# Kernel tuning notes

Hardware: AMD Instinct MI355X
Metric: run time of the kernel (lower is better)

## Reference

```python
import jax, jax.numpy as jnp
import numpy as np

B, C, H, W, K = 8, 256, 128, 128, 9
P = K // 2
DN = ('NCHW', 'OIHW', 'NCHW')


def _dw(x, w, pad):
    # depthwise conv: w has shape (C,1,kh,kw), feature_group_count=C
    return jax.lax.conv_general_dilated(
        x, w, window_strides=(1, 1), padding=pad,
        dimension_numbers=DN, feature_group_count=C)


def setup_inputs() -> dict:
    key = jax.random.key(0)
    ks = jax.random.split(key, 6)
    s = 1.0 / np.sqrt(K)
    return {
        'x': jax.random.normal(ks[0], (B, C, H, W), dtype=jnp.float32),
        'wh1': jax.random.normal(ks[1], (C, 1, 1, K), dtype=jnp.float32) * s,
        'wh2': jax.random.normal(ks[2], (C, 1, 1, K), dtype=jnp.float32) * s,
        'wv1': jax.random.normal(ks[3], (C, 1, K, 1), dtype=jnp.float32) * s,
        'wv2': jax.random.normal(ks[4], (C, 1, K, 1), dtype=jnp.float32) * s,
        'wproj': jax.random.normal(ks[5], (C, 4 * C), dtype=jnp.float32) / np.sqrt(4 * C),
    }


def reference(x, wh1, wh2, wv1, wv2, wproj):
    pad_h = ((0, 0), (P, P))  # 1xK conv pads width
    pad_v = ((P, P), (0, 0))  # Kx1 conv pads height
    y = jnp.concatenate([
        _dw(x, wh1, pad_h),
        _dw(x, wh2, pad_h),
        _dw(x, wv1, pad_v),
        _dw(x, wv2, pad_v),
    ], axis=1)  # (B, 4C, H, W)
    out = jnp.einsum('oc,bchw->bohw', wproj, y)  # 1x1 projection
    return jax.nn.relu(out)
```

## Files before the change

kernel.cpp:

```cpp
#include <hip/hip_runtime.h>
#include <hip/hip_bf16.h>

#define BB 8
#define CC 256
#define HH 128
#define WW 128
#define KS 9
#define NPIX (BB*HH*WW)
#define KDIM (4*CC)

#define XROW   2176
#define XT2_CG 295936
#define XT2_B  4734976
#define XT2_BYTES 75759616u

typedef __attribute__((ext_vector_type(8))) short bf16x8;
typedef __attribute__((ext_vector_type(4))) float f32x4;

static __device__ __forceinline__ unsigned short f2bf(float f) {
  union { float f; unsigned u; } v; v.f = f;
  unsigned r = v.u + 0x7FFF + ((v.u >> 16) & 1);
  return (unsigned short)(r >> 16);
}
static __device__ __forceinline__ float bf2f(unsigned short u) {
  union { unsigned u; float f; } v; v.u = ((unsigned)u) << 16;
  return v.f;
}

static __device__ __forceinline__ void gload_lds16(const void* g, void* l) {
  __builtin_amdgcn_global_load_lds(
      (const __attribute__((address_space(1))) void*)g,
      (__attribute__((address_space(3))) void*)l, 16, 0, 0);
}

__global__ void zero_kernel(uint4* __restrict__ p, long n16) {
  long i = (long)blockIdx.x * blockDim.x + threadIdx.x;
  long stride = (long)gridDim.x * blockDim.x;
  uint4 z = make_uint4(0, 0, 0, 0);
  for (; i < n16; i += stride) p[i] = z;
}

__global__ void prep_kernel(const float* __restrict__ wproj,
                            unsigned short* __restrict__ Ap) {
  int idx = blockIdx.x * 256 + threadIdx.x;
  int o  = idx >> 10;
  int kp = idx & 1023;
  int c  = kp >> 2;
  int t  = kp & 3;
  Ap[idx] = f2bf(wproj[o * 1024 + t * 256 + c]);
}

__global__ void wprep_kernel(const float* __restrict__ wh1,
                             const float* __restrict__ wh2,
                             const float* __restrict__ wv1,
                             const float* __restrict__ wv2,
                             float* __restrict__ wt) {
  int idx = blockIdx.x * 256 + threadIdx.x;
  int c = idx & 255;
  int q = idx >> 8;
  int cv = q / 9, k = q % 9;
  const float* src = (cv == 0) ? wh1 : (cv == 1) ? wh2 : (cv == 2) ? wv1 : wv2;
  wt[idx] = src[c * KS + k];
}

__global__ __launch_bounds__(256)
void transpose_kernel(const float* __restrict__ x,
                      unsigned short* __restrict__ xt2) {
  __shared__ float lds[64][65];
  int g   = blockIdx.x;
  int wt_ = g & 1;
  int h   = (g >> 1) & 127;
  int ct  = (g >> 8) & 3;
  int b   = g >> 10;
  int w0  = wt_ * 64;
  int tid = threadIdx.x;

  const float* xin = x + ((size_t)(b * 256 + ct * 64) << 14) + h * 128 + w0;
  int ci = tid >> 4;
  int w4 = (tid & 15) * 4;
#pragma unroll
  for (int i = 0; i < 4; ++i) {
    int c_ = ci + i * 16;
    float4 v = *(const float4*)(xin + ((size_t)c_ << 14) + w4);
    lds[c_][w4 + 0] = v.x; lds[c_][w4 + 1] = v.y;
    lds[c_][w4 + 2] = v.z; lds[c_][w4 + 3] = v.w;
  }
  __syncthreads();

  int wl  = (tid >> 6) * 16 + ((tid & 63) >> 2);
  int cl4 = (tid & 3) * 4;
#pragma unroll
  for (int g2 = 0; g2 < 4; ++g2) {
    ushort4 o;
    o.x = f2bf(lds[g2 * 16 + cl4 + 0][wl]);
    o.y = f2bf(lds[g2 * 16 + cl4 + 1][wl]);
    o.z = f2bf(lds[g2 * 16 + cl4 + 2][wl]);
    o.w = f2bf(lds[g2 * 16 + cl4 + 3][wl]);
    size_t dst = (size_t)b * XT2_B + (size_t)(ct * 4 + g2) * XT2_CG
               + (size_t)(h + 4) * XROW + (size_t)(w0 + wl + 4) * 16 + cl4;
    *(ushort4*)(xt2 + dst) = o;
  }
}

__global__ __launch_bounds__(512, 4)
void fused_kernel(const unsigned short* __restrict__ Ap,
                  const unsigned short* __restrict__ xt2,
                  const float* __restrict__ wt,
                  float* __restrict__ out) {
  __shared__ __align__(16) short Xs[9 * XROW];
  __shared__ __align__(16) short Bs[128 * 64];

  int bid = blockIdx.x;
  int pt  = (bid & 7) * 128 + (bid >> 3);
  int b   = pt >> 7, h = pt & 127;
  int tid = threadIdx.x;
  int lane = tid & 63;
  int wv  = tid >> 6;
  int om  = wv & 3, pn = wv >> 2;
  int l15 = lane & 15, kseg = lane >> 4;

  int cl = tid & 15;
  int wq = tid >> 4;

  const short* A  = (const short*)Ap;
  const short* xb = (const short*)xt2 + (size_t)b * XT2_B + (size_t)h * XROW;

  f32x4 acc[4][4] = {};

  for (int cg = 0; cg < 16; ++cg) {
    const char* src = (const char*)(xb + (size_t)cg * XT2_CG);
#pragma unroll
    for (int i = 0; i < 5; ++i) {
      int off = i * 8192 + tid * 16;
      if (off < 9 * XROW * 2)
        gload_lds16(src + off, (char*)Xs + off);
    }
    __syncthreads();

    bf16x8 af[2][4];
#pragma unroll
    for (int kk = 0; kk < 2; ++kk) {
      int kg = cg * 64 + kk * 32 + kseg * 8;
#pragma unroll
      for (int m = 0; m < 4; ++m)
        af[kk][m] = *(const bf16x8*)(A + (size_t)(om * 64 + m * 16 + l15) * KDIM + kg);
    }

    int c = cg * 16 + cl;
    float s[4][4];
#pragma unroll
    for (int dw = 0; dw < 4; ++dw)
#pragma unroll
      for (int t = 0; t < 4; ++t) s[dw][t] = 0.f;
#pragma unroll
    for (int j = 0; j < KS; ++j) {
      float w1 = wt[(0 * KS + j) * CC + c];
      float w2 = wt[(1 * KS + j) * CC + c];
      float w3 = wt[(2 * KS + j) * CC + c];
      float w4 = wt[(3 * KS + j) * CC + c];
#pragma unroll
      for (int dw = 0; dw < 4; ++dw) {
        int w = wq * 4 + dw;
        float xh = bf2f((unsigned short)Xs[4 * XROW + (w + j) * 16 + cl]);
        float xv = bf2f((unsigned short)Xs[j * XROW + (w + 4) * 16 + cl]);
        s[dw][0] = fmaf(xh, w1, s[dw][0]);
        s[dw][1] = fmaf(xh, w2, s[dw][1]);
        s[dw][2] = fmaf(xv, w3, s[dw][2]);
        s[dw][3] = fmaf(xv, w4, s[dw][3]);
      }
    }
#pragma unroll
    for (int dw = 0; dw < 4; ++dw) {
      int w = wq * 4 + dw;
      unsigned u0 = (unsigned)f2bf(s[dw][0]) | ((unsigned)f2bf(s[dw][1]) << 16);
      unsigned u1 = (unsigned)f2bf(s[dw][2]) | ((unsigned)f2bf(s[dw][3]) << 16);
      int byt = (w * 128 + cl * 8) ^ ((w & 7) << 4);
      *(uint2*)((char*)Bs + byt) = make_uint2(u0, u1);
    }
    __syncthreads();

#pragma unroll
    for (int kk = 0; kk < 2; ++kk) {
      bf16x8 bfr[4];
#pragma unroll
      for (int n = 0; n < 4; ++n) {
        int row = pn * 64 + n * 16 + l15;
        int byt = (row * 128 + kk * 64 + kseg * 16) ^ ((row & 7) << 4);
        bfr[n] = *(const bf16x8*)((const char*)Bs + byt);
      }
#pragma unroll
      for (int m = 0; m < 4; ++m)
#pragma unroll
        for (int n = 0; n < 4; ++n)
          acc[m][n] = __builtin_amdgcn_mfma_f32_16x16x32_bf16(af[kk][m], bfr[n],
                                                              acc[m][n], 0, 0, 0);
    }
    __syncthreads();
  }

  float* Ls = (float*)Xs;
  const int LP = 132;
  int b2 = pt >> 7, h2 = pt & 127;
  int er = tid >> 4;
  int ec = (tid & 15) * 8;
  size_t obase = ((size_t)(b2 * 256) << 14) + (h2 << 7);

#pragma unroll
  for (int oc = 0; oc < 8; ++oc) {
    __syncthreads();
    if (om == (oc >> 1)) {
      int mb = (oc & 1) * 2;
#pragma unroll
      for (int mm = 0; mm < 2; ++mm) {
#pragma unroll
        for (int n = 0; n < 4; ++n) {
#pragma unroll
          for (int r = 0; r < 4; ++r) {
            int row = mm * 16 + kseg * 4 + r;
            int col = pn * 64 + n * 16 + l15;
            Ls[row * LP + col] = acc[mb + mm][n][r];
          }
        }
      }
    }
    __syncthreads();
    float4 v0 = *(const float4*)&Ls[er * LP + ec];
    float4 v1 = *(const float4*)&Ls[er * LP + ec + 4];
    size_t oaddr = obase + ((size_t)(oc * 32 + er) << 14) + ec;
    *(float4*)&out[oaddr] = make_float4(fmaxf(v0.x, 0.f), fmaxf(v0.y, 0.f),
                                        fmaxf(v0.z, 0.f), fmaxf(v0.w, 0.f));
    *(float4*)&out[oaddr + 4] = make_float4(fmaxf(v1.x, 0.f), fmaxf(v1.y, 0.f),
                                            fmaxf(v1.z, 0.f), fmaxf(v1.w, 0.f));
  }
}

extern "C" void kernel_launch(void* const* d_in, const int* in_sizes, int n_in,
                              void* d_out, int out_size, void* d_ws, size_t ws_size,
                              hipStream_t stream) {
  (void)in_sizes; (void)n_in; (void)out_size; (void)ws_size;
  const float* x     = (const float*)d_in[0];
  const float* wh1   = (const float*)d_in[1];
  const float* wh2   = (const float*)d_in[2];
  const float* wv1   = (const float*)d_in[3];
  const float* wv2   = (const float*)d_in[4];
  const float* wproj = (const float*)d_in[5];
  float* out = (float*)d_out;

  char* wsb = (char*)d_ws;
  unsigned short* Xt2 = (unsigned short*)wsb;
  unsigned short* Ap  = (unsigned short*)(wsb + XT2_BYTES);
  float* Wt           = (float*)(wsb + XT2_BYTES + (size_t)CC * KDIM * 2);

  hipLaunchKernelGGL(zero_kernel, dim3(2048), dim3(256), 0, stream,
                     (uint4*)Xt2, (long)(XT2_BYTES / 16));
  hipLaunchKernelGGL(prep_kernel, dim3(1024), dim3(256), 0, stream, wproj, Ap);
  hipLaunchKernelGGL(wprep_kernel, dim3(36), dim3(256), 0, stream,
                     wh1, wh2, wv1, wv2, Wt);
  hipLaunchKernelGGL(transpose_kernel, dim3(8192), dim3(256), 0, stream, x, Xt2);
  hipLaunchKernelGGL(fused_kernel, dim3(1024), dim3(512), 0, stream,
                     Ap, Xt2, Wt, out);
}
```

Baseline: 541.9 us.

## Read fp32 input directly in fused kernel, dropping padded bf16 transpose staging

Removes the zero-fill and transpose kernels that built a padded channel-interleaved bf16 copy of x. The fused kernel now reads x straight from NCHW with float4 loads, handles halo boundaries with per-load bounds checks, and keeps the depthwise weights in LDS in per-channel order. This cuts a full extra pass over the input, the padded workspace writes and two kernel launches. In exchange each block reloads nine rows per channel from global memory through L2 instead of staging them once in LDS, and the per-thread loads are strided across channels, which may lower coalescing.

```diff
diff --git a/kernel.cpp b/kernel.cpp
--- a/kernel.cpp
+++ b/kernel.cpp
@@ -9,11 +9,6 @@
 #define NPIX (BB*HH*WW)
 #define KDIM (4*CC)
 
-#define XROW   2176
-#define XT2_CG 295936
-#define XT2_B  4734976
-#define XT2_BYTES 75759616u
-
 typedef __attribute__((ext_vector_type(8))) short bf16x8;
 typedef __attribute__((ext_vector_type(4))) float f32x4;
 
@@ -21,23 +16,6 @@
   union { float f; unsigned u; } v; v.f = f;
   unsigned r = v.u + 0x7FFF + ((v.u >> 16) & 1);
   return (unsigned short)(r >> 16);
-}
-static __device__ __forceinline__ float bf2f(unsigned short u) {
-  union { unsigned u; float f; } v; v.u = ((unsigned)u) << 16;
-  return v.f;
-}
-
-static __device__ __forceinline__ void gload_lds16(const void* g, void* l) {
-  __builtin_amdgcn_global_load_lds(
-      (const __attribute__((address_space(1))) void*)g,
-      (__attribute__((address_space(3))) void*)l, 16, 0, 0);
-}
-
-__global__ void zero_kernel(uint4* __restrict__ p, long n16) {
-  long i = (long)blockIdx.x * blockDim.x + threadIdx.x;
-  long stride = (long)gridDim.x * blockDim.x;
-  uint4 z = make_uint4(0, 0, 0, 0);
-  for (; i < n16; i += stride) p[i] = z;
 }
 
 __global__ void prep_kernel(const float* __restrict__ wproj,
@@ -54,60 +32,21 @@
                              const float* __restrict__ wh2,
                              const float* __restrict__ wv1,
                              const float* __restrict__ wv2,
-                             float* __restrict__ wt) {
+                             float* __restrict__ wt2) {
   int idx = blockIdx.x * 256 + threadIdx.x;
-  int c = idx & 255;
-  int q = idx >> 8;
-  int cv = q / 9, k = q % 9;
+  int c = idx / 36;
+  int q = idx - c * 36;
+  int cv = q / 9, k = q - cv * 9;
   const float* src = (cv == 0) ? wh1 : (cv == 1) ? wh2 : (cv == 2) ? wv1 : wv2;
-  wt[idx] = src[c * KS + k];
-}
-
-__global__ __launch_bounds__(256)
-void transpose_kernel(const float* __restrict__ x,
-                      unsigned short* __restrict__ xt2) {
-  __shared__ float lds[64][65];
-  int g   = blockIdx.x;
-  int wt_ = g & 1;
-  int h   = (g >> 1) & 127;
-  int ct  = (g >> 8) & 3;
-  int b   = g >> 10;
-  int w0  = wt_ * 64;
-  int tid = threadIdx.x;
-
-  const float* xin = x + ((size_t)(b * 256 + ct * 64) << 14) + h * 128 + w0;
-  int ci = tid >> 4;
-  int w4 = (tid & 15) * 4;
-#pragma unroll
-  for (int i = 0; i < 4; ++i) {
-    int c_ = ci + i * 16;
-    float4 v = *(const float4*)(xin + ((size_t)c_ << 14) + w4);
-    lds[c_][w4 + 0] = v.x; lds[c_][w4 + 1] = v.y;
-    lds[c_][w4 + 2] = v.z; lds[c_][w4 + 3] = v.w;
-  }
-  __syncthreads();
-
-  int wl  = (tid >> 6) * 16 + ((tid & 63) >> 2);
-  int cl4 = (tid & 3) * 4;
-#pragma unroll
-  for (int g2 = 0; g2 < 4; ++g2) {
-    ushort4 o;
-    o.x = f2bf(lds[g2 * 16 + cl4 + 0][wl]);
-    o.y = f2bf(lds[g2 * 16 + cl4 + 1][wl]);
-    o.z = f2bf(lds[g2 * 16 + cl4 + 2][wl]);
-    o.w = f2bf(lds[g2 * 16 + cl4 + 3][wl]);
-    size_t dst = (size_t)b * XT2_B + (size_t)(ct * 4 + g2) * XT2_CG
-               + (size_t)(h + 4) * XROW + (size_t)(w0 + wl + 4) * 16 + cl4;
-    *(ushort4*)(xt2 + dst) = o;
-  }
+  wt2[idx] = src[c * KS + k];
 }
 
 __global__ __launch_bounds__(512, 4)
 void fused_kernel(const unsigned short* __restrict__ Ap,
-                  const unsigned short* __restrict__ xt2,
-                  const float* __restrict__ wt,
+                  const float* __restrict__ x,
+                  const float* __restrict__ wt2,
                   float* __restrict__ out) {
-  __shared__ __align__(16) short Xs[9 * XROW];
+  __shared__ __align__(16) float Ws[256 * 36];
   __shared__ __align__(16) short Bs[128 * 64];
 
   int bid = blockIdx.x;
@@ -119,69 +58,83 @@
   int om  = wv & 3, pn = wv >> 2;
   int l15 = lane & 15, kseg = lane >> 4;
 
-  int cl = tid & 15;
-  int wq = tid >> 4;
-
+  int tc   = tid & 15;
+  int wseg = tid >> 4;
+  int w0   = wseg * 4;
+
+  {
+    const float4* srcw = (const float4*)wt2;
+    float4* dstw = (float4*)Ws;
+    for (int i = tid; i < 2304; i += 512) dstw[i] = srcw[i];
+  }
+  __syncthreads();
+
+  const float* xb = x + ((size_t)b << 22);
   const short* A  = (const short*)Ap;
-  const short* xb = (const short*)xt2 + (size_t)b * XT2_B + (size_t)h * XROW;
 
   f32x4 acc[4][4] = {};
 
   for (int cg = 0; cg < 16; ++cg) {
-    const char* src = (const char*)(xb + (size_t)cg * XT2_CG);
-#pragma unroll
-    for (int i = 0; i < 5; ++i) {
-      int off = i * 8192 + tid * 16;
-      if (off < 9 * XROW * 2)
-        gload_lds16(src + off, (char*)Xs + off);
-    }
-    __syncthreads();
-
-    bf16x8 af[2][4];
+    int c = cg * 16 + tc;
+    const float* xc = xb + ((size_t)c << 14);
+
+    float W[36];
+#pragma unroll
+    for (int i = 0; i < 9; ++i) {
+      float4 v = *(const float4*)&Ws[c * 36 + i * 4];
+      W[i*4+0] = v.x; W[i*4+1] = v.y; W[i*4+2] = v.z; W[i*4+3] = v.w;
+    }
+
+    float xh[12];
+    {
+      const float* xrow = xc + h * WW;
+#pragma unroll
+      for (int sgi = 0; sgi < 3; ++sgi) {
+        int wi = w0 - 4 + sgi * 4;
+        float4 v;
+        if (wi >= 0 && wi <= WW - 4) v = *(const float4*)(xrow + wi);
+        else v = make_float4(0.f, 0.f, 0.f, 0.f);
+        xh[sgi*4+0] = v.x; xh[sgi*4+1] = v.y;
+        xh[sgi*4+2] = v.z; xh[sgi*4+3] = v.w;
+      }
+    }
+
+    float s1[4] = {0.f,0.f,0.f,0.f}, s2[4] = {0.f,0.f,0.f,0.f};
+    float s3[4] = {0.f,0.f,0.f,0.f}, s4[4] = {0.f,0.f,0.f,0.f};
+#pragma unroll
+    for (int j = 0; j < KS; ++j) {
+      int r = h - 4 + j;
+      float4 vj;
+      if (r >= 0 && r < HH) vj = *(const float4*)(xc + r * WW + w0);
+      else vj = make_float4(0.f, 0.f, 0.f, 0.f);
+      float wj1 = W[j], wj2 = W[9+j], wj3 = W[18+j], wj4 = W[27+j];
+#pragma unroll
+      for (int dw = 0; dw < 4; ++dw) {
+        float a = xh[dw + j];
+        float v = (dw == 0) ? vj.x : (dw == 1) ? vj.y : (dw == 2) ? vj.z : vj.w;
+        s1[dw] = fmaf(a, wj1, s1[dw]);
+        s2[dw] = fmaf(a, wj2, s2[dw]);
+        s3[dw] = fmaf(v, wj3, s3[dw]);
+        s4[dw] = fmaf(v, wj4, s4[dw]);
+      }
+    }
+#pragma unroll
+    for (int dw = 0; dw < 4; ++dw) {
+      int w = w0 + dw;
+      unsigned u0 = (unsigned)f2bf(s1[dw]) | ((unsigned)f2bf(s2[dw]) << 16);
+      unsigned u1 = (unsigned)f2bf(s3[dw]) | ((unsigned)f2bf(s4[dw]) << 16);
+      int byt = (w * 128 + tc * 8) ^ ((w & 7) << 4);
+      *(uint2*)((char*)Bs + byt) = make_uint2(u0, u1);
+    }
+    __syncthreads();
+
 #pragma unroll
     for (int kk = 0; kk < 2; ++kk) {
+      bf16x8 af[4], bfr[4];
       int kg = cg * 64 + kk * 32 + kseg * 8;
 #pragma unroll
       for (int m = 0; m < 4; ++m)
-        af[kk][m] = *(const bf16x8*)(A + (size_t)(om * 64 + m * 16 + l15) * KDIM + kg);
-    }
-
-    int c = cg * 16 + cl;
-    float s[4][4];
-#pragma unroll
-    for (int dw = 0; dw < 4; ++dw)
-#pragma unroll
-      for (int t = 0; t < 4; ++t) s[dw][t] = 0.f;
-#pragma unroll
-    for (int j = 0; j < KS; ++j) {
-      float w1 = wt[(0 * KS + j) * CC + c];
-      float w2 = wt[(1 * KS + j) * CC + c];
-      float w3 = wt[(2 * KS + j) * CC + c];
-      float w4 = wt[(3 * KS + j) * CC + c];
-#pragma unroll
-      for (int dw = 0; dw < 4; ++dw) {
-        int w = wq * 4 + dw;
-        float xh = bf2f((unsigned short)Xs[4 * XROW + (w + j) * 16 + cl]);
-        float xv = bf2f((unsigned short)Xs[j * XROW + (w + 4) * 16 + cl]);
-        s[dw][0] = fmaf(xh, w1, s[dw][0]);
-        s[dw][1] = fmaf(xh, w2, s[dw][1]);
-        s[dw][2] = fmaf(xv, w3, s[dw][2]);
-        s[dw][3] = fmaf(xv, w4, s[dw][3]);
-      }
-    }
-#pragma unroll
-    for (int dw = 0; dw < 4; ++dw) {
-      int w = wq * 4 + dw;
-      unsigned u0 = (unsigned)f2bf(s[dw][0]) | ((unsigned)f2bf(s[dw][1]) << 16);
-      unsigned u1 = (unsigned)f2bf(s[dw][2]) | ((unsigned)f2bf(s[dw][3]) << 16);
-      int byt = (w * 128 + cl * 8) ^ ((w & 7) << 4);
-      *(uint2*)((char*)Bs + byt) = make_uint2(u0, u1);
-    }
-    __syncthreads();
-
-#pragma unroll
-    for (int kk = 0; kk < 2; ++kk) {
-      bf16x8 bfr[4];
+        af[m] = *(const bf16x8*)(A + (size_t)(om * 64 + m * 16 + l15) * KDIM + kg);
 #pragma unroll
       for (int n = 0; n < 4; ++n) {
         int row = pn * 64 + n * 16 + l15;
@@ -192,18 +145,17 @@
       for (int m = 0; m < 4; ++m)
 #pragma unroll
         for (int n = 0; n < 4; ++n)
-          acc[m][n] = __builtin_amdgcn_mfma_f32_16x16x32_bf16(af[kk][m], bfr[n],
+          acc[m][n] = __builtin_amdgcn_mfma_f32_16x16x32_bf16(af[m], bfr[n],
                                                               acc[m][n], 0, 0, 0);
     }
     __syncthreads();
   }
 
-  float* Ls = (float*)Xs;
+  float* Ls = (float*)Ws;
   const int LP = 132;
-  int b2 = pt >> 7, h2 = pt & 127;
   int er = tid >> 4;
   int ec = (tid & 15) * 8;
-  size_t obase = ((size_t)(b2 * 256) << 14) + (h2 << 7);
+  size_t obase = ((size_t)(b * 256) << 14) + (h << 7);
 
 #pragma unroll
   for (int oc = 0; oc < 8; ++oc) {
@@ -247,16 +199,12 @@
   float* out = (float*)d_out;
 
   char* wsb = (char*)d_ws;
-  unsigned short* Xt2 = (unsigned short*)wsb;
-  unsigned short* Ap  = (unsigned short*)(wsb + XT2_BYTES);
-  float* Wt           = (float*)(wsb + XT2_BYTES + (size_t)CC * KDIM * 2);
-
-  hipLaunchKernelGGL(zero_kernel, dim3(2048), dim3(256), 0, stream,
-                     (uint4*)Xt2, (long)(XT2_BYTES / 16));
+  unsigned short* Ap = (unsigned short*)wsb;
+  float* Wt2         = (float*)(wsb + (size_t)CC * KDIM * 2);
+
   hipLaunchKernelGGL(prep_kernel, dim3(1024), dim3(256), 0, stream, wproj, Ap);
   hipLaunchKernelGGL(wprep_kernel, dim3(36), dim3(256), 0, stream,
-                     wh1, wh2, wv1, wv2, Wt);
-  hipLaunchKernelGGL(transpose_kernel, dim3(8192), dim3(256), 0, stream, x, Xt2);
+                     wh1, wh2, wv1, wv2, Wt2);
   hipLaunchKernelGGL(fused_kernel, dim3(1024), dim3(512), 0, stream,
-                     Ap, Xt2, Wt, out);
-}
+                     Ap, x, Wt2, out);
+}
```

Result: slower. 1.073 ms (+98.0%).
